# Kernel tuning notes

Measured on AMD Instinct MI355X. Metric: run time of the kernel, lower is better.

The kernel has to match this reference:

```python
import jax, jax.numpy as jnp
import numpy as np

N_NODES = 100_000
N_EDGES = 1_000_000
H = 128
NUM_STATES = 4
UPPER_T, LOWER_T, NUM_ITERS, TEMP_EVAL = 1.0, 0.1, 10000, 0.1


def temp_by_step(step, upper, lower, num_iters, temp_eval):
    # Python-level schedule: eval temp at step == -1, else linear anneal.
    if step == -1:
        return temp_eval
    frac = min(step / num_iters, 1.0)
    return upper + (lower - upper) * frac


def from_binary_states(states):
    # [*, k] bits -> integer id in [0, 2**k)
    weights = 2 ** jnp.arange(states.shape[-1])
    return (states * weights).sum(-1)


def setup_inputs() -> dict:
    key = jax.random.key(0)
    ks = jax.random.split(key, 20)
    N, E, h = N_NODES, N_EDGES, H
    node_states = jax.random.randint(ks[0], (N, NUM_STATES), 0, 2)
    edge_states = jax.random.randint(ks[1], (E, NUM_STATES), 0, 2)
    scalars = jax.random.normal(ks[2], (E, 1), jnp.float32)
    # first N edges are self-loops ordered by node id (required by the module's
    # node_scalars = scalars[src == dst] indexing convention)
    loops = jnp.arange(N)
    src = jax.random.randint(ks[3], (E - N,), 0, N)
    dst = jax.random.randint(ks[4], (E - N,), 0, N)
    dst = jnp.where(dst == src, (dst + 1) % N, dst)  # no accidental self-loops
    edge_index = jnp.stack([jnp.concatenate([loops, src]),
                            jnp.concatenate([loops, dst])])
    batched_reverse_idx = jax.random.randint(ks[5], (E,), 0, E)
    batch_scalars = jax.random.normal(ks[6], (E, 1, 1), jnp.float32)
    s = 0.02
    params = dict(
        node_emb=s * jax.random.normal(ks[7], (2 ** NUM_STATES, h), jnp.float32),
        edge_emb=s * jax.random.normal(ks[8], (2 ** NUM_STATES, h), jnp.float32),
        combine_W=s * jax.random.normal(ks[9], (2 * h, h), jnp.float32),
        combine_b=jnp.zeros((h,), jnp.float32),
        keep_W=s * jax.random.normal(ks[10], (h, 2), jnp.float32),
        keep_b=jnp.zeros((2,), jnp.float32),
        push_W=s * jax.random.normal(ks[11], (h, 2), jnp.float32),
        push_b=jnp.zeros((2,), jnp.float32),
        push_node_W=s * jax.random.normal(ks[12], (h, 2), jnp.float32),
        push_node_b=jnp.zeros((2,), jnp.float32),
        increment_W=s * jax.random.normal(ks[13], (h, 2), jnp.float32),
        increment_b=jnp.zeros((2,), jnp.float32),
    )
    return dict(node_states=node_states, edge_states=edge_states, scalars=scalars,
                edge_index=edge_index, batched_reverse_idx=batched_reverse_idx,
                batch_scalars=batch_scalars, processor_step=0, training_step=0,
                **params)


def reference(node_states, edge_states, scalars, edge_index, batched_reverse_idx,
              batch_scalars, processor_step, training_step,
              node_emb, edge_emb, combine_W, combine_b, keep_W, keep_b,
              push_W, push_b, push_node_W, push_node_b,
              increment_W, increment_b):
    N = node_states.shape[0]
    tau = temp_by_step(int(training_step), UPPER_T, LOWER_T, NUM_ITERS, TEMP_EVAL)
    # use_noise = config.use_noise (False) and training_step != -1 -> False

    node_fts = node_emb[from_binary_states(node_states)]   # [N, h]
    edge_fts = edge_emb[from_binary_states(edge_states)]   # [E, h]
    src, dst = edge_index[0], edge_index[1]
    fts = jnp.concatenate([edge_fts[batched_reverse_idx], node_fts[src]], axis=1)
    fts = fts @ combine_W + combine_b                       # [E, h]

    s = scalars.reshape(-1)                                 # [E]

    def pair_gumbel_first(W, b):
        # grouped (per-edge pair) softmax; take first component (== [::2])
        logits = (fts @ W + b) / tau                        # [E, 2]
        return jax.nn.softmax(logits, axis=-1)[:, 0]

    increment = 1.0 * pair_gumbel_first(increment_W, increment_b)
    keep = s * pair_gumbel_first(keep_W, keep_b)

    # push: first N edges are self-loops, self-loop of node i is edge i
    push_wo = pair_gumbel_first(push_W, push_b)
    push_w = pair_gumbel_first(push_node_W, push_node_b)
    node_scalars = s[:N]                                    # scalars at self-loops
    s_wo = s - node_scalars[dst]
    s_w = s_wo + node_scalars[src]
    acc = (jax.ops.segment_sum(push_wo * s_wo, dst, num_segments=N)
           + jax.ops.segment_sum(push_w * s_w, dst, num_segments=N))  # [N]
    edge_push = jnp.zeros_like(s).at[:N].set(acc)           # nonzero only on self-loops

    new_scalars = (increment + keep + edge_push)[:, None]   # [E, 1]
    target = batch_scalars[:, processor_step]               # [E, 1]
    loss = jnp.mean((target - new_scalars) ** 2)
    return new_scalars, loss
```

## Files before the change

kernel.cpp:

```cpp
#include <hip/hip_runtime.h>
#include <math.h>

#define N_NODES 100000
#define N_EDGES 1000000
#define HDIM 128

typedef float vfloat4 __attribute__((ext_vector_type(4)));

__device__ __forceinline__ float get_invtau(const int* __restrict__ training_step) {
    int step = training_step[0];
    float tau;
    if (step == -1) {
        tau = 0.1f;
    } else {
        float frac = fminf((float)step / 10000.0f, 1.0f);
        tau = 1.0f + (0.1f - 1.0f) * frac;
    }
    return 1.0f / tau;
}

__device__ __forceinline__ float wave_reduce(float v) {
    #pragma unroll
    for (int off = 32; off > 0; off >>= 1) v += __shfl_down(v, off, 64);
    return v;
}

__global__ void tab_stage1(const float* __restrict__ cW,
                           const float* __restrict__ kW, const float* __restrict__ pW,
                           const float* __restrict__ pnW, const float* __restrict__ iW,
                           const int* __restrict__ tstep,
                           float* __restrict__ uv)
{
    __shared__ float wd[512];
    const float invtau = get_invtau(tstep);
    for (int i = threadIdx.x; i < 512; i += 256) {
        const int h = i >> 7, d = i & 127;
        const float* W = (h == 0) ? kW : (h == 1) ? pW : (h == 2) ? pnW : iW;
        wd[i] = W[2 * d] - W[2 * d + 1];
    }
    __syncthreads();

    const int row  = blockIdx.x * 4 + (threadIdx.x >> 6);
    const int lane = threadIdx.x & 63;
    const int half = row >> 9;
    const int r    = row & 511;
    const int h    = r >> 7, d = r & 127;
    const int cwrow = half * 128 + d;

    float p = cW[cwrow * 128 + lane]      * wd[h * 128 + lane]
            + cW[cwrow * 128 + 64 + lane] * wd[h * 128 + 64 + lane];
    p = wave_reduce(p);
    if (lane == 0) uv[row] = p * invtau;
}

__global__ void tab_stage2(const float* __restrict__ node_emb,
                           const float* __restrict__ edge_emb,
                           const float* __restrict__ cb,
                           const float* __restrict__ kW, const float* __restrict__ kb,
                           const float* __restrict__ pW, const float* __restrict__ pb,
                           const float* __restrict__ pnW, const float* __restrict__ pnb,
                           const float* __restrict__ iW, const float* __restrict__ ib,
                           const int* __restrict__ tstep,
                           const float* __restrict__ uv,
                           float* __restrict__ tabs)
{
    const int w = blockIdx.x * 4 + (threadIdx.x >> 6);
    if (w >= 132) return;
    const int lane = threadIdx.x & 63;
    const float invtau = get_invtau(tstep);

    float p;
    if (w < 128) {
        const int isB = w >> 6, h = (w >> 4) & 3, i = w & 15;
        const float* emb = isB ? node_emb : edge_emb;
        const float* uvp = uv + isB * 512 + h * 128;
        p = emb[i * 128 + lane] * uvp[lane] + emb[i * 128 + 64 + lane] * uvp[64 + lane];
    } else {
        const int h = w - 128;
        const float* W = (h == 0) ? kW : (h == 1) ? pW : (h == 2) ? pnW : iW;
        p = cb[lane]      * (W[2 * lane] - W[2 * lane + 1])
          + cb[64 + lane] * (W[2 * (64 + lane)] - W[2 * (64 + lane) + 1]);
    }
    p = wave_reduce(p);
    if (lane == 0) {
        if (w < 64) {
            const int h = (w >> 4) & 3, i = w & 15;
            tabs[i * 4 + h] = p;
        } else if (w < 128) {
            const int h = (w >> 4) & 3, i = w & 15;
            tabs[64 + i * 4 + h] = p;
        } else {
            const int h = w - 128;
            const float* b = (h == 0) ? kb : (h == 1) ? pb : (h == 2) ? pnb : ib;
            tabs[128 + h] = (p + b[0] - b[1]) * invtau;
        }
    }
}

__global__ void precompute(const int* __restrict__ node_states,
                           const int* __restrict__ edge_states,
                           unsigned char* __restrict__ es_idx,
                           unsigned char* __restrict__ ns_idx,
                           float* __restrict__ acc,
                           float* __restrict__ loss_out)
{
    const int e = blockIdx.x * blockDim.x + threadIdx.x;
    if (e < N_EDGES) {
        int4 st = ((const int4*)edge_states)[e];
        es_idx[e] = (unsigned char)(st.x + 2 * st.y + 4 * st.z + 8 * st.w);
    }
    if (e < N_NODES) {
        int4 st = ((const int4*)node_states)[e];
        ns_idx[e] = (unsigned char)(st.x + 2 * st.y + 4 * st.z + 8 * st.w);
        acc[e] = 0.f;
    }
    if (e == 0) *loss_out = 0.f;
}

__global__ __launch_bounds__(256) void edge_kernel(
    const float* __restrict__ s,
    const int* __restrict__ src,
    const int* __restrict__ dst,
    const int* __restrict__ brev,
    const unsigned char* __restrict__ es_idx,
    const unsigned char* __restrict__ ns_idx,
    const float* __restrict__ tabs,
    const float* __restrict__ target,
    float* __restrict__ acc,
    float* __restrict__ out,
    float* __restrict__ loss_out)
{
    __shared__ float4 sf[33];
    if (threadIdx.x < 33) sf[threadIdx.x] = ((const float4*)tabs)[threadIdx.x];
    __syncthreads();

    const int t = blockIdx.x * blockDim.x + threadIdx.x;
    const int e0 = t * 4;
    float lsum = 0.f;

    if (e0 < N_EDGES) {
        const int4   rv = ((const int4*)brev)[t];
        const int4   sr = ((const int4*)src)[t];
        const int4   ds = ((const int4*)dst)[t];
        const float4 sv = ((const float4*)s)[t];
        const vfloat4 tg = __builtin_nontemporal_load(&((const vfloat4*)target)[t]);

        const int rvv[4] = {rv.x, rv.y, rv.z, rv.w};
        const int srv[4] = {sr.x, sr.y, sr.z, sr.w};
        const int dsv[4] = {ds.x, ds.y, ds.z, ds.w};
        const float svv[4] = {sv.x, sv.y, sv.z, sv.w};
        const float tgv[4] = {tg.x, tg.y, tg.z, tg.w};

        int ei[4], ni[4];
        float sd[4], ss[4];
        #pragma unroll
        for (int j = 0; j < 4; ++j) {
            ei[j] = es_idx[rvv[j]];
            ni[j] = ns_idx[srv[j]];
            sd[j] = s[dsv[j]];
            ss[j] = s[srv[j]];
        }

        const float4 c4 = sf[32];
        float ov[4];
        #pragma unroll
        for (int j = 0; j < 4; ++j) {
            const float4 a = sf[ei[j]];
            const float4 b = sf[16 + ni[j]];
            const float lk  = a.x + b.x + c4.x;
            const float lp  = a.y + b.y + c4.y;
            const float lpn = a.z + b.z + c4.z;
            const float li  = a.w + b.w + c4.w;
            const float pk  = 1.f / (1.f + __expf(-lk));
            const float pp  = 1.f / (1.f + __expf(-lp));
            const float ppn = 1.f / (1.f + __expf(-lpn));
            const float pi  = 1.f / (1.f + __expf(-li));

            const float s_wo = svv[j] - sd[j];
            const float s_w  = s_wo + ss[j];
            atomicAdd(&acc[dsv[j]], pp * s_wo + ppn * s_w);

            ov[j] = pi + svv[j] * pk;
            if (e0 + j >= N_NODES) {
                const float d = tgv[j] - ov[j];
                lsum += d * d;
            }
        }
        vfloat4 o4 = {ov[0], ov[1], ov[2], ov[3]};
        __builtin_nontemporal_store(o4, &((vfloat4*)out)[t]);
    }

    lsum = wave_reduce(lsum);
    __shared__ float wsum[4];
    const int lane = threadIdx.x & 63, wid = threadIdx.x >> 6;
    if (lane == 0) wsum[wid] = lsum;
    __syncthreads();
    if (threadIdx.x == 0) {
        const float tot = wsum[0] + wsum[1] + wsum[2] + wsum[3];
        atomicAdd(loss_out, tot * (1.0f / (float)N_EDGES));
    }
}

__global__ void finalize_nodes(const float* __restrict__ target,
                               const float* __restrict__ acc,
                               float* __restrict__ out,
                               float* __restrict__ loss_out)
{
    const int e = blockIdx.x * blockDim.x + threadIdx.x;
    float sq = 0.f;
    if (e < N_NODES) {
        const float v = out[e] + acc[e];
        out[e] = v;
        const float d = target[e] - v;
        sq = d * d;
    }
    sq = wave_reduce(sq);
    __shared__ float wsum[4];
    const int lane = threadIdx.x & 63, wid = threadIdx.x >> 6;
    if (lane == 0) wsum[wid] = sq;
    __syncthreads();
    if (threadIdx.x == 0) {
        const float tot = wsum[0] + wsum[1] + wsum[2] + wsum[3];
        atomicAdd(loss_out, tot * (1.0f / (float)N_EDGES));
    }
}

extern "C" void kernel_launch(void* const* d_in, const int* in_sizes, int n_in,
                              void* d_out, int out_size, void* d_ws, size_t ws_size,
                              hipStream_t stream) {
    const int*   node_states   = (const int*)d_in[0];
    const int*   edge_states   = (const int*)d_in[1];
    const float* scalars       = (const float*)d_in[2];
    const int*   edge_index    = (const int*)d_in[3];
    const int*   brev          = (const int*)d_in[4];
    const float* batch_scalars = (const float*)d_in[5];
    const int*   training_step = (const int*)d_in[7];
    const float* node_emb  = (const float*)d_in[8];
    const float* edge_emb  = (const float*)d_in[9];
    const float* combine_W = (const float*)d_in[10];
    const float* combine_b = (const float*)d_in[11];
    const float* keep_W  = (const float*)d_in[12];
    const float* keep_b  = (const float*)d_in[13];
    const float* push_W  = (const float*)d_in[14];
    const float* push_b  = (const float*)d_in[15];
    const float* pushn_W = (const float*)d_in[16];
    const float* pushn_b = (const float*)d_in[17];
    const float* inc_W   = (const float*)d_in[18];
    const float* inc_b   = (const float*)d_in[19];

    float* out = (float*)d_out;

    char* ws = (char*)d_ws;
    float* tabs = (float*)ws;
    float* uv   = (float*)(ws + 1024);
    float* acc  = (float*)(ws + 1024 + 4096);
    unsigned char* es_idx = (unsigned char*)(ws + 1024 + 4096 + (size_t)N_NODES * 4);
    unsigned char* ns_idx = es_idx + N_EDGES;

    const int* srcp = edge_index;
    const int* dstp = edge_index + N_EDGES;

    tab_stage1<<<256, 256, 0, stream>>>(combine_W, keep_W, push_W, pushn_W, inc_W,
                                        training_step, uv);
    tab_stage2<<<33, 256, 0, stream>>>(node_emb, edge_emb, combine_b,
                                       keep_W, keep_b, push_W, push_b,
                                       pushn_W, pushn_b, inc_W, inc_b,
                                       training_step, uv, tabs);

    precompute<<<(N_EDGES + 255) / 256, 256, 0, stream>>>(node_states, edge_states,
                                                          es_idx, ns_idx, acc,
                                                          out + N_EDGES);

    const int ethreads = N_EDGES / 4;
    edge_kernel<<<(ethreads + 255) / 256, 256, 0, stream>>>(
        scalars, srcp, dstp, brev, es_idx, ns_idx, tabs, batch_scalars,
        acc, out, out + N_EDGES);

    finalize_nodes<<<(N_NODES + 255) / 256, 256, 0, stream>>>(
        batch_scalars, acc, out, out + N_EDGES);
}
```

Before: 186.3 us.

## Specialize self-loop edges in node finalize kernel, skip their gathers and atomics

The edge kernel now handles only the non-self-loop edges, two per thread. The self-loop edges are computed directly in the node finalize kernel, which uses the known identities src=dst=n for them, so their scalar gathers and atomic adds to acc are no longer needed. Atomics switch to unsafeAtomicAdd, allowing hardware float atomics, and the per-element self-loop branch in the loss is removed. The cost is narrower vector loads and more threads in the edge kernel, plus extra table work in finalize.

```diff
diff --git a/kernel.cpp b/kernel.cpp
--- a/kernel.cpp
+++ b/kernel.cpp
@@ -4,8 +4,10 @@
 #define N_NODES 100000
 #define N_EDGES 1000000
 #define HDIM 128
-
-typedef float vfloat4 __attribute__((ext_vector_type(4)));
+#define N_NONLOOP (N_EDGES - N_NODES)
+
+typedef float  vfloat2 __attribute__((ext_vector_type(2)));
+typedef float  vfloat4 __attribute__((ext_vector_type(4)));
 
 __device__ __forceinline__ float get_invtau(const int* __restrict__ training_step) {
     int step = training_step[0];
@@ -135,26 +137,26 @@
     __syncthreads();
 
     const int t = blockIdx.x * blockDim.x + threadIdx.x;
-    const int e0 = t * 4;
     float lsum = 0.f;
 
-    if (e0 < N_EDGES) {
-        const int4   rv = ((const int4*)brev)[t];
-        const int4   sr = ((const int4*)src)[t];
-        const int4   ds = ((const int4*)dst)[t];
-        const float4 sv = ((const float4*)s)[t];
-        const vfloat4 tg = __builtin_nontemporal_load(&((const vfloat4*)target)[t]);
-
-        const int rvv[4] = {rv.x, rv.y, rv.z, rv.w};
-        const int srv[4] = {sr.x, sr.y, sr.z, sr.w};
-        const int dsv[4] = {ds.x, ds.y, ds.z, ds.w};
-        const float svv[4] = {sv.x, sv.y, sv.z, sv.w};
-        const float tgv[4] = {tg.x, tg.y, tg.z, tg.w};
-
-        int ei[4], ni[4];
-        float sd[4], ss[4];
+    if (t < N_NONLOOP / 2) {
+        const int g = (N_NODES / 2) + t;
+        const int2   rv = ((const int2*)brev)[g];
+        const int2   sr = ((const int2*)src)[g];
+        const int2   ds = ((const int2*)dst)[g];
+        const float2 sv = ((const float2*)s)[g];
+        const float2 tg = ((const float2*)target)[g];
+
+        const int rvv[2] = {rv.x, rv.y};
+        const int srv[2] = {sr.x, sr.y};
+        const int dsv[2] = {ds.x, ds.y};
+        const float svv[2] = {sv.x, sv.y};
+        const float tgv[2] = {tg.x, tg.y};
+
+        int ei[2], ni[2];
+        float sd[2], ss[2];
         #pragma unroll
-        for (int j = 0; j < 4; ++j) {
+        for (int j = 0; j < 2; ++j) {
             ei[j] = es_idx[rvv[j]];
             ni[j] = ns_idx[srv[j]];
             sd[j] = s[dsv[j]];
@@ -162,9 +164,9 @@
         }
 
         const float4 c4 = sf[32];
-        float ov[4];
+        float ov[2];
         #pragma unroll
-        for (int j = 0; j < 4; ++j) {
+        for (int j = 0; j < 2; ++j) {
             const float4 a = sf[ei[j]];
             const float4 b = sf[16 + ni[j]];
             const float lk  = a.x + b.x + c4.x;
@@ -178,16 +180,14 @@
 
             const float s_wo = svv[j] - sd[j];
             const float s_w  = s_wo + ss[j];
-            atomicAdd(&acc[dsv[j]], pp * s_wo + ppn * s_w);
+            unsafeAtomicAdd(&acc[dsv[j]], pp * s_wo + ppn * s_w);
 
             ov[j] = pi + svv[j] * pk;
-            if (e0 + j >= N_NODES) {
-                const float d = tgv[j] - ov[j];
-                lsum += d * d;
-            }
+            const float d = tgv[j] - ov[j];
+            lsum += d * d;
         }
-        vfloat4 o4 = {ov[0], ov[1], ov[2], ov[3]};
-        __builtin_nontemporal_store(o4, &((vfloat4*)out)[t]);
+        vfloat2 o2 = {ov[0], ov[1]};
+        __builtin_nontemporal_store(o2, &((vfloat2*)out)[g]);
     }
 
     lsum = wave_reduce(lsum);
@@ -201,17 +201,42 @@
     }
 }
 
-__global__ void finalize_nodes(const float* __restrict__ target,
-                               const float* __restrict__ acc,
-                               float* __restrict__ out,
-                               float* __restrict__ loss_out)
-{
-    const int e = blockIdx.x * blockDim.x + threadIdx.x;
+__global__ __launch_bounds__(256) void finalize_nodes(
+    const float* __restrict__ s,
+    const int* __restrict__ brev,
+    const unsigned char* __restrict__ es_idx,
+    const unsigned char* __restrict__ ns_idx,
+    const float* __restrict__ tabs,
+    const float* __restrict__ target,
+    const float* __restrict__ acc,
+    float* __restrict__ out,
+    float* __restrict__ loss_out)
+{
+    __shared__ float4 sf[33];
+    if (threadIdx.x < 33) sf[threadIdx.x] = ((const float4*)tabs)[threadIdx.x];
+    __syncthreads();
+
+    const int n = blockIdx.x * blockDim.x + threadIdx.x;
     float sq = 0.f;
-    if (e < N_NODES) {
-        const float v = out[e] + acc[e];
-        out[e] = v;
-        const float d = target[e] - v;
+    if (n < N_NODES) {
+        const int   rev = brev[n];
+        const int   ei  = es_idx[rev];
+        const int   ni  = ns_idx[n];
+        const float sv  = s[n];
+
+        const float4 a = sf[ei];
+        const float4 b = sf[16 + ni];
+        const float4 c4 = sf[32];
+        const float lk  = a.x + b.x + c4.x;
+        const float lpn = a.z + b.z + c4.z;
+        const float li  = a.w + b.w + c4.w;
+        const float pk  = 1.f / (1.f + __expf(-lk));
+        const float ppn = 1.f / (1.f + __expf(-lpn));
+        const float pi  = 1.f / (1.f + __expf(-li));
+
+        const float v = pi + sv * pk + ppn * sv + acc[n];
+        out[n] = v;
+        const float d = target[n] - v;
         sq = d * d;
     }
     sq = wave_reduce(sq);
@@ -271,11 +296,11 @@
                                                           es_idx, ns_idx, acc,
                                                           out + N_EDGES);
 
-    const int ethreads = N_EDGES / 4;
+    const int ethreads = N_NONLOOP / 2;
     edge_kernel<<<(ethreads + 255) / 256, 256, 0, stream>>>(
         scalars, srcp, dstp, brev, es_idx, ns_idx, tabs, batch_scalars,
         acc, out, out + N_EDGES);
 
     finalize_nodes<<<(N_NODES + 255) / 256, 256, 0, stream>>>(
-        batch_scalars, acc, out, out + N_EDGES);
-}
+        scalars, brev, es_idx, ns_idx, tabs, batch_scalars, acc, out, out + N_EDGES);
+}
```

After: 184.2 us. About the same (-1.1%).
